# Optimization experiments

Hardware: AMD Instinct MI355X
Metric: run time of the kernel (lower is better)

Reference implementation:

```python
import jax, jax.numpy as jnp
import numpy as np

SEQ, BATCH, IN_F, STATE, OUT_F = 2048, 32, 256, 512, 256


def setup_inputs() -> dict:
    key = jax.random.key(0)
    k1, k2, k3, k4 = jax.random.split(key, 4)
    x = jax.random.normal(k1, (SEQ, BATCH, IN_F), dtype=jnp.float32)
    # lambda_log init per module __init__ with rmin=0, rmax=1:
    # u ~ U(0,1); lambda_log = log(-0.5*log(u*(rmax+rmin)*(rmax-rmin)+rmin^2)) = log(-0.5*log(u))
    u = jax.random.uniform(k2, (STATE,), dtype=jnp.float32, minval=1e-6, maxval=1.0)
    lambda_log = jnp.log(-0.5 * jnp.log(u))
    B = jax.random.normal(k3, (STATE, IN_F), dtype=jnp.float32) / np.float32(np.sqrt(IN_F))
    C = jax.random.normal(k4, (OUT_F, STATE), dtype=jnp.float32) / np.float32(np.sqrt(STATE))
    return {"input": x, "lambda_log": lambda_log, "B": B, "C": C}


def reference(input, lambda_log, B, C):
    # mode='sequential', inner_loops=1, rnn_burnin=0, done=None, hidden=None
    lamda = jnp.exp(-jnp.exp(lambda_log))                 # [N]
    gamma = jnp.sqrt(1.0 - lamda * lamda + 1e-7)          # [N]
    # project all timesteps at once: b_seq[s,b,n] = gamma_n * (x_s @ B^T)
    b_seq = jnp.einsum('sbi,ni->sbn', input, B) * gamma   # [S,B,N]

    def step(state, b_t):
        new_state = lamda * state + b_t                   # diagonal LRU recurrence
        return new_state, new_state

    init = jnp.zeros((input.shape[1], lambda_log.shape[0]), dtype=input.dtype)
    final_state, states = jax.lax.scan(step, init, b_seq)  # states: [S,B,N]
    output = jnp.einsum('sbn,on->sbo', states, C)          # [S,B,O]
    return output, final_state
```

## Files before the change

kernel.cpp:

```cpp
#include <hip/hip_runtime.h>

#define SEQ   2048
#define BATCH 32
#define INF   256
#define NST   512
#define OUTF  256
#define CLEN  32
#define NCH   64
#define NJOB  4
#define NCG   (NCH / NJOB)
#define NBLK  (NCG * BATCH)

typedef __bf16 bf16;
typedef __bf16 bf16x8 __attribute__((ext_vector_type(8)));
typedef float  f32x4  __attribute__((ext_vector_type(4)));

__global__ void k_prep(const float* __restrict__ ll,
                       const float* __restrict__ Bm,
                       const float* __restrict__ Cm,
                       float* __restrict__ lam,
                       float* __restrict__ lamG,
                       float* __restrict__ l2la,
                       bf16* __restrict__ Bb,
                       bf16* __restrict__ Cb) {
  int i = blockIdx.x * 256 + threadIdx.x;
  if (i < NST) {
    float e = expf(ll[i]);
    float lmb = expf(-e);
    lam[i] = lmb;
    l2la[i] = -e * 1.44269504088896341f;
    float p = lmb;
#pragma unroll
    for (int q = 0; q < 7; ++q) p *= p;
    lamG[i] = p;
  }
  if (i < NST * INF) {
    int n = i >> 8;
    float lmb = expf(-expf(ll[n]));
    float g = sqrtf(1.0f - lmb * lmb + 1e-7f);
    Bb[i] = (bf16)(Bm[i] * g);
  }
  if (i < OUTF * NST) {
    Cb[i] = (bf16)(Cm[i]);
  }
}

__device__ __forceinline__ void xload(const float* __restrict__ xp, int tid,
                                      float4 xr[4]) {
#pragma unroll
  for (int rep = 0; rep < 4; ++rep) {
    int slot = rep * 512 + tid;
    int row = slot >> 6, col4 = slot & 63;
    xr[rep] = *(const float4*)(xp + (size_t)row * (BATCH * INF) + col4 * 4);
  }
}

__device__ __forceinline__ void xstore(char* xsb, int tid, const float4 xr[4]) {
#pragma unroll
  for (int rep = 0; rep < 4; ++rep) {
    int slot = rep * 512 + tid;
    int row = slot >> 6, col4 = slot & 63;
    union { bf16 h[4]; unsigned long long u; } pk;
    pk.h[0] = (bf16)xr[rep].x; pk.h[1] = (bf16)xr[rep].y;
    pk.h[2] = (bf16)xr[rep].z; pk.h[3] = (bf16)xr[rep].w;
    int byte = (row * (INF * 2) + col4 * 8) ^ ((row & 15) << 4);
    *(unsigned long long*)(xsb + byte) = pk.u;
  }
}

__device__ __forceinline__ void reg_scan(f32x4 acc[2][4], float carry[4],
                                         const float la[4], const float l4[4],
                                         int kg, int rl) {
#pragma unroll
  for (int mt = 0; mt < 2; ++mt) {
    float sl[4][4];
#pragma unroll
    for (int nt = 0; nt < 4; ++nt) {
      sl[nt][0] = acc[mt][nt][0];
      sl[nt][1] = fmaf(la[nt], sl[nt][0], acc[mt][nt][1]);
      sl[nt][2] = fmaf(la[nt], sl[nt][1], acc[mt][nt][2]);
      sl[nt][3] = fmaf(la[nt], sl[nt][2], acc[mt][nt][3]);
    }
    float G[4];
#pragma unroll
    for (int nt = 0; nt < 4; ++nt) {
      float g1 = __shfl_up(sl[nt][3], 16);
      G[nt] = (kg >= 1) ? fmaf(l4[nt], g1, sl[nt][3]) : sl[nt][3];
    }
#pragma unroll
    for (int nt = 0; nt < 4; ++nt) {
      float l8 = l4[nt] * l4[nt];
      float g2 = __shfl_up(G[nt], 32);
      G[nt] = (kg >= 2) ? fmaf(l8, g2, G[nt]) : G[nt];
    }
#pragma unroll
    for (int nt = 0; nt < 4; ++nt) {
      float X = __shfl_up(G[nt], 16);
      X = (kg >= 1) ? X : 0.0f;
      float l8 = l4[nt] * l4[nt];
      float p4k = ((kg & 1) ? l4[nt] : 1.0f) * ((kg & 2) ? l8 : 1.0f);
      float cin = fmaf(p4k, carry[nt], X);
      float l2 = la[nt] * la[nt], l3 = l2 * la[nt];
      acc[mt][nt][0] = fmaf(la[nt], cin, sl[nt][0]);
      acc[mt][nt][1] = fmaf(l2, cin, sl[nt][1]);
      acc[mt][nt][2] = fmaf(l3, cin, sl[nt][2]);
      acc[mt][nt][3] = fmaf(l4[nt], cin, sl[nt][3]);
    }
#pragma unroll
    for (int nt = 0; nt < 4; ++nt)
      carry[nt] = __shfl(acc[mt][nt][3], rl + 48);
  }
}

__device__ __forceinline__ void gemm1_breg(const char* xsb, const bf16x8 Breg[8][4],
                                           f32x4 acc[2][4], int rl, int kg) {
#pragma unroll
  for (int k = 0; k < 8; ++k) {
    bf16x8 af[2];
#pragma unroll
    for (int mt = 0; mt < 2; ++mt) {
      int row = mt * 16 + rl;
      int byte = (row * (INF * 2) + (k * 32 + kg * 8) * 2) ^ (rl << 4);
      af[mt] = *(const bf16x8*)(xsb + byte);
    }
#pragma unroll
    for (int mt = 0; mt < 2; ++mt)
#pragma unroll
      for (int nt = 0; nt < 4; ++nt)
        acc[mt][nt] = __builtin_amdgcn_mfma_f32_16x16x32_bf16(af[mt], Breg[k][nt], acc[mt][nt], 0, 0, 0);
  }
}

__device__ __forceinline__ void gemm1_l2(const char* xsb, const bf16* __restrict__ Bb,
                                         f32x4 acc[2][4], int n0, int rl, int kg) {
#pragma unroll
  for (int k = 0; k < 8; ++k) {
    bf16x8 af[2], bfr[4];
#pragma unroll
    for (int mt = 0; mt < 2; ++mt) {
      int row = mt * 16 + rl;
      int byte = (row * (INF * 2) + (k * 32 + kg * 8) * 2) ^ (rl << 4);
      af[mt] = *(const bf16x8*)(xsb + byte);
    }
#pragma unroll
    for (int nt = 0; nt < 4; ++nt)
      bfr[nt] = *(const bf16x8*)(Bb + (size_t)(n0 + nt * 16 + rl) * INF + k * 32 + kg * 8);
#pragma unroll
    for (int mt = 0; mt < 2; ++mt)
#pragma unroll
      for (int nt = 0; nt < 4; ++nt)
        acc[mt][nt] = __builtin_amdgcn_mfma_f32_16x16x32_bf16(af[mt], bfr[nt], acc[mt][nt], 0, 0, 0);
  }
}

template <int STORE>
__global__ __launch_bounds__(512, 2)
void k_pass0(const float* __restrict__ x, const bf16* __restrict__ Bb,
             const float* __restrict__ lam, float* __restrict__ Z,
             bf16* __restrict__ bfrag) {
  __shared__ __align__(16) char xs[2][CLEN * INF * 2];

  const int tid = threadIdx.x, wid = tid >> 6, lane = tid & 63;
  const int rl = lane & 15, kg = lane >> 4;
  const int b = blockIdx.x >> 4, cg = blockIdx.x & 15;
  const int n0 = wid * 64;

  float la[4], l4[4], carry[4];
#pragma unroll
  for (int nt = 0; nt < 4; ++nt) {
    float v = lam[n0 + nt * 16 + rl];
    la[nt] = v; l4[nt] = (v * v) * (v * v);
    carry[nt] = 0.0f;
  }

  bf16x8 Breg[8][4];
#pragma unroll
  for (int k = 0; k < 8; ++k)
#pragma unroll
    for (int nt = 0; nt < 4; ++nt)
      Breg[k][nt] = *(const bf16x8*)(Bb + (size_t)(n0 + nt * 16 + rl) * INF + k * 32 + kg * 8);

  {
    float4 xr0[4];
    xload(x + ((size_t)(cg * NJOB * CLEN) * BATCH + b) * INF, tid, xr0);
    xstore(xs[0], tid, xr0);
  }
  __syncthreads();

#pragma unroll
  for (int jj = 0; jj < NJOB; ++jj) {
    const int c = cg * NJOB + jj;
    f32x4 acc[2][4] = {};
    gemm1_breg(&xs[jj & 1][0], Breg, acc, rl, kg);

    float4 xr[4];
    if (jj < NJOB - 1)
      xload(x + ((size_t)((c + 1) * CLEN) * BATCH + b) * INF, tid, xr);

    reg_scan(acc, carry, la, l4, kg, rl);

    if (STORE) {
      const size_t rowbase = ((size_t)cg * BATCH + b) * 128 + jj * 32;
#pragma unroll
      for (int mt = 0; mt < 2; ++mt)
#pragma unroll
        for (int nt = 0; nt < 4; ++nt)
#pragma unroll
          for (int r = 0; r < 4; ++r) {
            int t = mt * 16 + kg * 4 + r;
            int n = n0 + nt * 16 + rl;
            bfrag[(rowbase + t) * NST + n] = (bf16)acc[mt][nt][r];
          }
    }

    if (jj < NJOB - 1) {
      xstore(xs[(jj + 1) & 1], tid, xr);
      __syncthreads();
    } else {
      if (kg == 0)
#pragma unroll
        for (int nt = 0; nt < 4; ++nt)
          Z[((size_t)cg * BATCH + b) * NST + n0 + nt * 16 + rl] = carry[nt];
    }
  }
}

__global__ __launch_bounds__(128)
void k_chain(const float* __restrict__ Z, const float* __restrict__ lamG,
             float* __restrict__ S0, float* __restrict__ fin) {
  const int b = blockIdx.x;
  const int n = blockIdx.y * 128 + threadIdx.x;
  const float lG = lamG[n];
  float z[NCG];
#pragma unroll
  for (int g = 0; g < NCG; ++g)
    z[g] = Z[((size_t)g * BATCH + b) * NST + n];
  float s = 0.0f;
#pragma unroll
  for (int g = 0; g < NCG; ++g) {
    S0[((size_t)g * BATCH + b) * NST + n] = s;
    s = fmaf(lG, s, z[g]);
  }
  fin[(size_t)b * NST + n] = s;
}

__global__ __launch_bounds__(512)
void k_gemm2b(const bf16* __restrict__ bfrag, const bf16* __restrict__ Cb,
              const float* __restrict__ S0, const float* __restrict__ l2la,
              float* __restrict__ out) {
  __shared__ __align__(16) char ss[64 * NST * 2];

  const int tid = threadIdx.x, wid = tid >> 6, lane = tid & 63;
  const int rl = lane & 15, kg = lane >> 4;
  const int c2 = blockIdx.x >> 5, b = blockIdx.x & 31;
  const int cg = c2 >> 1;
  const int dtbase = (c2 & 1) * 64;

  const int n8 = (tid & 63) * 8;
  float l2a[8], s0g[8];
#pragma unroll
  for (int j = 0; j < 8; ++j) {
    l2a[j] = l2la[n8 + j];
    s0g[j] = S0[((size_t)cg * BATCH + b) * NST + n8 + j];
  }

  const uint4* src = (const uint4*)(bfrag +
      (((size_t)cg * BATCH + b) * 128 + dtbase) * NST);
#pragma unroll
  for (int q = 0; q < 8; ++q) {
    int chunk = q * 512 + tid;
    int tl = chunk >> 6;
    union { uint4 u; bf16 h[8]; } in, ot;
    in.u = src[chunk];
    float dtp1 = (float)(dtbase + tl + 1);
#pragma unroll
    for (int j = 0; j < 8; ++j) {
      float s = fmaf(exp2f(dtp1 * l2a[j]), s0g[j], (float)in.h[j]);
      ot.h[j] = (bf16)s;
    }
    int byte = (tl * (NST * 2) + (chunk & 63) * 16) ^ ((tl & 15) << 4);
    *(uint4*)(&ss[0] + byte) = ot.u;
  }
  __syncthreads();

  const int o0 = wid * 32;
  f32x4 acc[4][2] = {};
#pragma unroll
  for (int kq = 0; kq < 16; ++kq) {
    const int k0 = kq * 32;
    bf16x8 af[4], cf[2];
#pragma unroll
    for (int mf = 0; mf < 4; ++mf) {
      int t = mf * 16 + rl;
      af[mf] = *(const bf16x8*)(&ss[0] +
          ((t * (NST * 2) + (k0 + kg * 8) * 2) ^ ((t & 15) << 4)));
    }
#pragma unroll
    for (int ot2 = 0; ot2 < 2; ++ot2)
      cf[ot2] = *(const bf16x8*)(Cb + (size_t)(o0 + ot2 * 16 + rl) * NST + k0 + kg * 8);
#pragma unroll
    for (int mf = 0; mf < 4; ++mf)
#pragma unroll
      for (int ot2 = 0; ot2 < 2; ++ot2)
        acc[mf][ot2] = __builtin_amdgcn_mfma_f32_16x16x32_bf16(af[mf], cf[ot2], acc[mf][ot2], 0, 0, 0);
  }

#pragma unroll
  for (int mf = 0; mf < 4; ++mf)
#pragma unroll
    for (int ot2 = 0; ot2 < 2; ++ot2)
#pragma unroll
      for (int r = 0; r < 4; ++r) {
        int ml = mf * 16 + kg * 4 + r;
        size_t srow = (size_t)c2 * 64 + ml;
        int o = o0 + ot2 * 16 + rl;
        out[(srow * BATCH + b) * OUTF + o] = acc[mf][ot2][r];
      }
}

__global__ __launch_bounds__(512)
void k_pass1_fb(const float* __restrict__ x, const bf16* __restrict__ Bb,
                const bf16* __restrict__ Cb, const float* __restrict__ lam,
                const float* __restrict__ S0, float* __restrict__ out,
                float* __restrict__ fin) {
  __shared__ __align__(16) char xs[2][CLEN * INF * 2];
  __shared__ __align__(16) char ss[CLEN * NST * 2];

  const int tid = threadIdx.x, wid = tid >> 6, lane = tid & 63;
  const int rl = lane & 15, kg = lane >> 4;
  const int b = blockIdx.x >> 4, cg = blockIdx.x & 15;
  const int n0 = wid * 64;

  float la[4], l4[4], carry[4];
#pragma unroll
  for (int nt = 0; nt < 4; ++nt) {
    float v = lam[n0 + nt * 16 + rl];
    la[nt] = v; l4[nt] = (v * v) * (v * v);
    carry[nt] = S0[((size_t)cg * BATCH + b) * NST + n0 + nt * 16 + rl];
  }
  {
    float4 xr0[4];
    xload(x + ((size_t)(cg * NJOB * CLEN) * BATCH + b) * INF, tid, xr0);
    xstore(xs[0], tid, xr0);
  }
  __syncthreads();

#pragma unroll
  for (int jj = 0; jj < NJOB; ++jj) {
    const int c = cg * NJOB + jj;
    f32x4 acc[2][4] = {};
    gemm1_l2(&xs[jj & 1][0], Bb, acc, n0, rl, kg);
    {
      float4 xr[4];
      const int lastj = (jj == NJOB - 1);
      if (!lastj)
        xload(x + ((size_t)((c + 1) * CLEN) * BATCH + b) * INF, tid, xr);
      reg_scan(acc, carry, la, l4, kg, rl);
      if (c == NCH - 1 && kg == 0)
#pragma unroll
        for (int nt = 0; nt < 4; ++nt)
          fin[(size_t)b * NST + n0 + nt * 16 + rl] = carry[nt];
      __syncthreads();
#pragma unroll
      for (int mt = 0; mt < 2; ++mt)
#pragma unroll
        for (int nt = 0; nt < 4; ++nt)
#pragma unroll
          for (int r = 0; r < 4; ++r) {
            int t = mt * 16 + kg * 4 + r;
            int n = n0 + nt * 16 + rl;
            int byte = (t * (NST * 2) + n * 2) ^ ((t & 15) << 4);
            *(bf16*)(&ss[0] + byte) = (bf16)acc[mt][nt][r];
          }
      if (!lastj) xstore(xs[(jj + 1) & 1], tid, xr);
    }
    __syncthreads();

    const int o0 = wid * 32;
    f32x4 a2[2][2] = {};
#pragma unroll
    for (int k0 = 0; k0 < NST; k0 += 32) {
      bf16x8 af[2], cf[2];
#pragma unroll
      for (int mt = 0; mt < 2; ++mt) {
        int t = mt * 16 + rl;
        int byte = (t * (NST * 2) + (k0 + kg * 8) * 2) ^ (rl << 4);
        af[mt] = *(const bf16x8*)(&ss[0] + byte);
      }
#pragma unroll
      for (int ot = 0; ot < 2; ++ot)
        cf[ot] = *(const bf16x8*)(Cb + (size_t)(o0 + ot * 16 + rl) * NST + k0 + kg * 8);
#pragma unroll
      for (int mt = 0; mt < 2; ++mt)
#pragma unroll
        for (int ot = 0; ot < 2; ++ot)
          a2[mt][ot] = __builtin_amdgcn_mfma_f32_16x16x32_bf16(af[mt], cf[ot], a2[mt][ot], 0, 0, 0);
    }
#pragma unroll
    for (int mt = 0; mt < 2; ++mt)
#pragma unroll
      for (int ot = 0; ot < 2; ++ot)
#pragma unroll
        for (int r = 0; r < 4; ++r) {
          int t = mt * 16 + kg * 4 + r;
          int o = o0 + ot * 16 + rl;
          out[(((size_t)(c * CLEN + t)) * BATCH + b) * OUTF + o] = a2[mt][ot][r];
        }
  }
}

extern "C" void kernel_launch(void* const* d_in, const int* in_sizes, int n_in,
                              void* d_out, int out_size, void* d_ws, size_t ws_size,
                              hipStream_t stream) {
  const float* x  = (const float*)d_in[0];
  const float* ll = (const float*)d_in[1];
  const float* Bm = (const float*)d_in[2];
  const float* Cm = (const float*)d_in[3];

  char* ws = (char*)d_ws;
  float* lam  = (float*)(ws);
  float* lamG = (float*)(ws + 2048);
  float* l2la = (float*)(ws + 4096);
  bf16*  Bb   = (bf16*)(ws + 6144);
  bf16*  Cb   = (bf16*)(ws + 6144 + NST * INF * 2);
  float* Z    = (float*)(ws + 6144 + NST * INF * 2 + OUTF * NST * 2);
  float* S0   = (float*)((char*)Z + (size_t)NCG * BATCH * NST * 4);
  bf16*  bfrag= (bf16*)((char*)S0 + (size_t)NCG * BATCH * NST * 4);
  const size_t NEED = ((char*)bfrag - ws) + (size_t)SEQ * BATCH * NST * 2;

  float* out = (float*)d_out;
  float* fin = out + (size_t)SEQ * BATCH * OUTF;

  k_prep<<<dim3(512), dim3(256), 0, stream>>>(ll, Bm, Cm, lam, lamG, l2la, Bb, Cb);
  if (ws_size >= NEED) {
    k_pass0<1><<<dim3(NBLK), dim3(512), 0, stream>>>(x, Bb, lam, Z, bfrag);
    k_chain<<<dim3(BATCH, 4), dim3(128), 0, stream>>>(Z, lamG, S0, fin);
    k_gemm2b<<<dim3(1024), dim3(512), 0, stream>>>(bfrag, Cb, S0, l2la, out);
  } else {
    k_pass0<0><<<dim3(NBLK), dim3(512), 0, stream>>>(x, Bb, lam, Z, bfrag);
    k_chain<<<dim3(BATCH, 4), dim3(128), 0, stream>>>(Z, lamG, S0, fin);
    k_pass1_fb<<<dim3(NBLK), dim3(512), 0, stream>>>(x, Bb, Cb, lam, S0, out, fin);
  }
}
```

Baseline: 98.77 us.

## Transpose pass0 MFMA output so time lies along lanes and store packed bf16

The main pass0 kernel swaps the MFMA operands so each lane holds four state channels for one timestep. The chunk scan becomes a log-step shuffle scan across the 16 lanes of each group instead of the previous register/group scan. This lets the bf16 state fragments be written as 8-byte packed stores and the chunk carries as float4 stores, replacing many scattered 2-byte stores. The shuffle scan adds more cross-lane operations, the launch_bounds min-blocks hint is dropped, and the old templated kernel is split into a separate fallback kernel.

```diff
diff --git a/kernel.cpp b/kernel.cpp
--- a/kernel.cpp
+++ b/kernel.cpp
@@ -112,11 +112,11 @@
   }
 }
 
-__device__ __forceinline__ void gemm1_breg(const char* xsb, const bf16x8 Breg[8][4],
-                                           f32x4 acc[2][4], int rl, int kg) {
+__device__ __forceinline__ void gemm1_l2(const char* xsb, const bf16* __restrict__ Bb,
+                                         f32x4 acc[2][4], int n0, int rl, int kg) {
 #pragma unroll
   for (int k = 0; k < 8; ++k) {
-    bf16x8 af[2];
+    bf16x8 af[2], bfr[4];
 #pragma unroll
     for (int mt = 0; mt < 2; ++mt) {
       int row = mt * 16 + rl;
@@ -124,25 +124,6 @@
       af[mt] = *(const bf16x8*)(xsb + byte);
     }
 #pragma unroll
-    for (int mt = 0; mt < 2; ++mt)
-#pragma unroll
-      for (int nt = 0; nt < 4; ++nt)
-        acc[mt][nt] = __builtin_amdgcn_mfma_f32_16x16x32_bf16(af[mt], Breg[k][nt], acc[mt][nt], 0, 0, 0);
-  }
-}
-
-__device__ __forceinline__ void gemm1_l2(const char* xsb, const bf16* __restrict__ Bb,
-                                         f32x4 acc[2][4], int n0, int rl, int kg) {
-#pragma unroll
-  for (int k = 0; k < 8; ++k) {
-    bf16x8 af[2], bfr[4];
-#pragma unroll
-    for (int mt = 0; mt < 2; ++mt) {
-      int row = mt * 16 + rl;
-      int byte = (row * (INF * 2) + (k * 32 + kg * 8) * 2) ^ (rl << 4);
-      af[mt] = *(const bf16x8*)(xsb + byte);
-    }
-#pragma unroll
     for (int nt = 0; nt < 4; ++nt)
       bfr[nt] = *(const bf16x8*)(Bb + (size_t)(n0 + nt * 16 + rl) * INF + k * 32 + kg * 8);
 #pragma unroll
@@ -153,25 +134,26 @@
   }
 }
 
-template <int STORE>
-__global__ __launch_bounds__(512, 2)
-void k_pass0(const float* __restrict__ x, const bf16* __restrict__ Bb,
-             const float* __restrict__ lam, float* __restrict__ Z,
-             bf16* __restrict__ bfrag) {
+__global__ __launch_bounds__(512)
+void k_pass0s(const float* __restrict__ x, const bf16* __restrict__ Bb,
+              const float* __restrict__ lam, float* __restrict__ Z,
+              bf16* __restrict__ bfrag) {
   __shared__ __align__(16) char xs[2][CLEN * INF * 2];
 
   const int tid = threadIdx.x, wid = tid >> 6, lane = tid & 63;
   const int rl = lane & 15, kg = lane >> 4;
   const int b = blockIdx.x >> 4, cg = blockIdx.x & 15;
   const int n0 = wid * 64;
-
-  float la[4], l4[4], carry[4];
-#pragma unroll
-  for (int nt = 0; nt < 4; ++nt) {
-    float v = lam[n0 + nt * 16 + rl];
-    la[nt] = v; l4[nt] = (v * v) * (v * v);
-    carry[nt] = 0.0f;
-  }
+  const int seg15 = (lane & 48) | 15;
+
+  float la2[4][4], carry2[4][4];
+#pragma unroll
+  for (int nt = 0; nt < 4; ++nt)
+#pragma unroll
+    for (int r = 0; r < 4; ++r) {
+      la2[nt][r] = lam[n0 + nt * 16 + kg * 4 + r];
+      carry2[nt][r] = 0.0f;
+    }
 
   bf16x8 Breg[8][4];
 #pragma unroll
@@ -190,37 +172,84 @@
 #pragma unroll
   for (int jj = 0; jj < NJOB; ++jj) {
     const int c = cg * NJOB + jj;
+
     f32x4 acc[2][4] = {};
-    gemm1_breg(&xs[jj & 1][0], Breg, acc, rl, kg);
+#pragma unroll
+    for (int k = 0; k < 8; ++k) {
+      bf16x8 af[2];
+#pragma unroll
+      for (int mt = 0; mt < 2; ++mt) {
+        int row = mt * 16 + rl;
+        int byte = (row * (INF * 2) + (k * 32 + kg * 8) * 2) ^ (rl << 4);
+        af[mt] = *(const bf16x8*)(&xs[jj & 1][0] + byte);
+      }
+#pragma unroll
+      for (int mt = 0; mt < 2; ++mt)
+#pragma unroll
+        for (int nt = 0; nt < 4; ++nt)
+          acc[mt][nt] = __builtin_amdgcn_mfma_f32_16x16x32_bf16(Breg[k][nt], af[mt], acc[mt][nt], 0, 0, 0);
+    }
 
     float4 xr[4];
     if (jj < NJOB - 1)
       xload(x + ((size_t)((c + 1) * CLEN) * BATCH + b) * INF, tid, xr);
 
-    reg_scan(acc, carry, la, l4, kg, rl);
-
-    if (STORE) {
+#pragma unroll
+    for (int nt = 0; nt < 4; ++nt)
+#pragma unroll
+      for (int r = 0; r < 4; ++r) {
+        const float la = la2[nt][r];
+        float v0 = acc[0][nt][r];
+        v0 = (rl == 0) ? fmaf(la, carry2[nt][r], v0) : v0;
+        float w = la;
+#pragma unroll
+        for (int d = 1; d <= 8; d <<= 1) {
+          float u = __shfl_up(v0, d);
+          v0 = (rl >= d) ? fmaf(w, u, v0) : v0;
+          w = w * w;
+        }
+        float c0 = __shfl(v0, seg15);
+        float v1 = acc[1][nt][r];
+        v1 = (rl == 0) ? fmaf(la, c0, v1) : v1;
+        w = la;
+#pragma unroll
+        for (int d = 1; d <= 8; d <<= 1) {
+          float u = __shfl_up(v1, d);
+          v1 = (rl >= d) ? fmaf(w, u, v1) : v1;
+          w = w * w;
+        }
+        carry2[nt][r] = __shfl(v1, seg15);
+        acc[0][nt][r] = v0;
+        acc[1][nt][r] = v1;
+      }
+
+    {
       const size_t rowbase = ((size_t)cg * BATCH + b) * 128 + jj * 32;
 #pragma unroll
       for (int mt = 0; mt < 2; ++mt)
 #pragma unroll
-        for (int nt = 0; nt < 4; ++nt)
-#pragma unroll
-          for (int r = 0; r < 4; ++r) {
-            int t = mt * 16 + kg * 4 + r;
-            int n = n0 + nt * 16 + rl;
-            bfrag[(rowbase + t) * NST + n] = (bf16)acc[mt][nt][r];
-          }
+        for (int nt = 0; nt < 4; ++nt) {
+          union { bf16 h[4]; unsigned long long u; } pk;
+          pk.h[0] = (bf16)acc[mt][nt][0];
+          pk.h[1] = (bf16)acc[mt][nt][1];
+          pk.h[2] = (bf16)acc[mt][nt][2];
+          pk.h[3] = (bf16)acc[mt][nt][3];
+          size_t row = rowbase + mt * 16 + rl;
+          *(unsigned long long*)(bfrag + row * NST + n0 + nt * 16 + kg * 4) = pk.u;
+        }
     }
 
     if (jj < NJOB - 1) {
       xstore(xs[(jj + 1) & 1], tid, xr);
       __syncthreads();
     } else {
-      if (kg == 0)
-#pragma unroll
-        for (int nt = 0; nt < 4; ++nt)
-          Z[((size_t)cg * BATCH + b) * NST + n0 + nt * 16 + rl] = carry[nt];
+      if (rl == 15)
+#pragma unroll
+        for (int nt = 0; nt < 4; ++nt) {
+          float4 zv = make_float4(carry2[nt][0], carry2[nt][1],
+                                  carry2[nt][2], carry2[nt][3]);
+          *(float4*)(Z + ((size_t)cg * BATCH + b) * NST + n0 + nt * 16 + kg * 4) = zv;
+        }
     }
   }
 }
@@ -316,6 +345,74 @@
         int o = o0 + ot2 * 16 + rl;
         out[(srow * BATCH + b) * OUTF + o] = acc[mf][ot2][r];
       }
+}
+
+__global__ __launch_bounds__(512, 2)
+void k_pass0_fb(const float* __restrict__ x, const bf16* __restrict__ Bb,
+                const float* __restrict__ lam, float* __restrict__ Z) {
+  __shared__ __align__(16) char xs[2][CLEN * INF * 2];
+
+  const int tid = threadIdx.x, wid = tid >> 6, lane = tid & 63;
+  const int rl = lane & 15, kg = lane >> 4;
+  const int b = blockIdx.x >> 4, cg = blockIdx.x & 15;
+  const int n0 = wid * 64;
+
+  float la[4], l4[4], carry[4];
+#pragma unroll
+  for (int nt = 0; nt < 4; ++nt) {
+    float v = lam[n0 + nt * 16 + rl];
+    la[nt] = v; l4[nt] = (v * v) * (v * v);
+    carry[nt] = 0.0f;
+  }
+
+  bf16x8 Breg[8][4];
+#pragma unroll
+  for (int k = 0; k < 8; ++k)
+#pragma unroll
+    for (int nt = 0; nt < 4; ++nt)
+      Breg[k][nt] = *(const bf16x8*)(Bb + (size_t)(n0 + nt * 16 + rl) * INF + k * 32 + kg * 8);
+
+  {
+    float4 xr0[4];
+    xload(x + ((size_t)(cg * NJOB * CLEN) * BATCH + b) * INF, tid, xr0);
+    xstore(xs[0], tid, xr0);
+  }
+  __syncthreads();
+
+#pragma unroll
+  for (int jj = 0; jj < NJOB; ++jj) {
+    const int c = cg * NJOB + jj;
+    f32x4 acc[2][4] = {};
+#pragma unroll
+    for (int k = 0; k < 8; ++k) {
+      bf16x8 af[2];
+#pragma unroll
+      for (int mt = 0; mt < 2; ++mt) {
+        int row = mt * 16 + rl;
+        int byte = (row * (INF * 2) + (k * 32 + kg * 8) * 2) ^ (rl << 4);
+        af[mt] = *(const bf16x8*)(&xs[jj & 1][0] + byte);
+      }
+#pragma unroll
+      for (int mt = 0; mt < 2; ++mt)
+#pragma unroll
+        for (int nt = 0; nt < 4; ++nt)
+          acc[mt][nt] = __builtin_amdgcn_mfma_f32_16x16x32_bf16(af[mt], Breg[k][nt], acc[mt][nt], 0, 0, 0);
+    }
+
+    if (jj < NJOB - 1) {
+      float4 xr[4];
+      xload(x + ((size_t)((c + 1) * CLEN) * BATCH + b) * INF, tid, xr);
+      reg_scan(acc, carry, la, l4, kg, rl);
+      xstore(xs[(jj + 1) & 1], tid, xr);
+      __syncthreads();
+    } else {
+      reg_scan(acc, carry, la, l4, kg, rl);
+      if (kg == 0)
+#pragma unroll
+        for (int nt = 0; nt < 4; ++nt)
+          Z[((size_t)cg * BATCH + b) * NST + n0 + nt * 16 + rl] = carry[nt];
+    }
+  }
 }
 
 __global__ __launch_bounds__(512)
@@ -433,11 +530,11 @@
 
   k_prep<<<dim3(512), dim3(256), 0, stream>>>(ll, Bm, Cm, lam, lamG, l2la, Bb, Cb);
   if (ws_size >= NEED) {
-    k_pass0<1><<<dim3(NBLK), dim3(512), 0, stream>>>(x, Bb, lam, Z, bfrag);
+    k_pass0s<<<dim3(NBLK), dim3(512), 0, stream>>>(x, Bb, lam, Z, bfrag);
     k_chain<<<dim3(BATCH, 4), dim3(128), 0, stream>>>(Z, lamG, S0, fin);
     k_gemm2b<<<dim3(1024), dim3(512), 0, stream>>>(bfrag, Cb, S0, l2la, out);
   } else {
-    k_pass0<0><<<dim3(NBLK), dim3(512), 0, stream>>>(x, Bb, lam, Z, bfrag);
+    k_pass0_fb<<<dim3(NBLK), dim3(512), 0, stream>>>(x, Bb, lam, Z);
     k_chain<<<dim3(BATCH, 4), dim3(128), 0, stream>>>(Z, lamG, S0, fin);
     k_pass1_fb<<<dim3(NBLK), dim3(512), 0, stream>>>(x, Bb, Cb, lam, S0, out, fin);
   }
```

Result: slower. 186.9 us (+89.2%).
